# Performance work log

Measured on AMD Instinct MI355X. Metric: run time of the kernel, lower is better.

The kernel has to match this reference:

```python
import jax, jax.numpy as jnp
import numpy as np

EMBED_DIM = 1024
N_HEADS = 16
HEAD_DIM = EMBED_DIM // N_HEADS

def setup_inputs() -> dict:
    key = jax.random.key(0)
    kx, kq, kk, kv, ko = jax.random.split(key, 5)
    s = 1.0 / np.sqrt(EMBED_DIM)
    return {
        "x": jax.random.normal(kx, (4, 2048, EMBED_DIM), dtype=jnp.float32),
        "Wq": jax.random.normal(kq, (EMBED_DIM, EMBED_DIM), dtype=jnp.float32) * s,
        "Wk": jax.random.normal(kk, (EMBED_DIM, EMBED_DIM), dtype=jnp.float32) * s,
        "Wv": jax.random.normal(kv, (EMBED_DIM, EMBED_DIM), dtype=jnp.float32) * s,
        "Wo": jax.random.normal(ko, (EMBED_DIM, EMBED_DIM), dtype=jnp.float32) * s,
    }

def reference(x, Wq, Wk, Wv, Wo):
    B, T, D = x.shape
    H, Dh = N_HEADS, HEAD_DIM
    # projections (nn.Linear: y = x @ W.T); split heads -> [B, H, T, Dh]
    Q = (x @ Wq.T).reshape(B, T, H, Dh).transpose(0, 2, 1, 3)
    K = (x @ Wk.T).reshape(B, T, H, Dh).transpose(0, 2, 1, 3)
    V = (x @ Wv.T).reshape(B, T, H, Dh).transpose(0, 2, 1, 3)
    scores = jnp.einsum("bhqd,bhkd->bhqk", Q, K) / jnp.sqrt(jnp.float32(Dh))
    attn = jax.nn.softmax(scores, axis=-1)
    out = jnp.einsum("bhqk,bhkd->bhqd", attn, V)  # [B,H,T,Dh]
    out = out.transpose(0, 2, 1, 3).reshape(B, T, D)
    return out @ Wo.T
```

## Files before the change

### kernel.cpp

```cpp
#include <hip/hip_runtime.h>

typedef _Float16 f16;
typedef _Float16 f16x8 __attribute__((ext_vector_type(8)));
typedef _Float16 f16x4 __attribute__((ext_vector_type(4)));
typedef float f32x4 __attribute__((ext_vector_type(4)));

#define MFMA16(a, b, c) __builtin_amdgcn_mfma_f32_16x16x32_f16((a), (b), (c), 0, 0, 0)
#define MEMBAR() __asm__ __volatile__("" ::: "memory")

__device__ __forceinline__ void cp16(const f16* g, f16* l) {
  __builtin_amdgcn_global_load_lds(
      (const __attribute__((address_space(1))) void*)g,
      (__attribute__((address_space(3))) void*)l, 16, 0, 0);
}

__global__ __launch_bounds__(256) void cvt_all(
    const float* __restrict__ x,  const float* __restrict__ Wq,
    const float* __restrict__ Wk, const float* __restrict__ Wv,
    const float* __restrict__ Wo,
    f16* __restrict__ X16, f16* __restrict__ Wq16, f16* __restrict__ Wk16,
    f16* __restrict__ Wv16, f16* __restrict__ Wo16) {
  int blk = blockIdx.x;
  const float* src; f16* dst; size_t off;
  if (blk < 4096) { src = x; dst = X16; off = (size_t)blk * 2048; }
  else {
    int t = blk - 4096, widx = t >> 9, loc = t & 511;
    src = (widx == 0) ? Wq : (widx == 1) ? Wk : (widx == 2) ? Wv : Wo;
    dst = (widx == 0) ? Wq16 : (widx == 1) ? Wk16 : (widx == 2) ? Wv16 : Wo16;
    off = (size_t)loc * 2048;
  }
  size_t e = off + (size_t)threadIdx.x * 8;
  const float4* s = (const float4*)(src + e);
  float4 a = s[0], b = s[1];
  f16x8 o;
  o[0] = (f16)a.x; o[1] = (f16)a.y; o[2] = (f16)a.z; o[3] = (f16)a.w;
  o[4] = (f16)b.x; o[5] = (f16)b.y; o[6] = (f16)b.z; o[7] = (f16)b.w;
  *(f16x8*)(dst + e) = o;
}

__device__ __forceinline__ void gemm_core(
    const f16* __restrict__ A, const f16* __restrict__ B, void* __restrict__ Cv,
    bool outF16, bool permT, int N, int K, int bm, int bn, float scale,
    f16* As, f16* Bs) {
  const int tid = threadIdx.x;
  const int lane = tid & 63, w = tid >> 6;
  const int wm = w >> 1, wn = w & 1;
  const int c = lane & 15, q = lane >> 4;
  const int key = (c >> 1) & 3;
  f32x4 acc[4][4] = {};

  const int Lrow = lane >> 2, Lp = (lane & 3) ^ ((lane >> 3) & 3);
  auto stage = [&](int k0, int bufi) {
#pragma unroll
    for (int j = 0; j < 2; ++j) {
      int r0 = (w * 2 + j) * 16;
      cp16(A + (size_t)(bm + r0 + Lrow) * K + k0 + Lp * 8,
           As + bufi * 4096 + r0 * 32 + lane * 8);
    }
#pragma unroll
    for (int j = 0; j < 2; ++j) {
      int r0 = (w * 2 + j) * 16;
      cp16(B + (size_t)(bn + r0 + Lrow) * K + k0 + Lp * 8,
           Bs + bufi * 4096 + r0 * 32 + lane * 8);
    }
  };

  stage(0, 0);
  const int NIT = K >> 5;
  for (int i = 0; i < NIT; ++i) {
    if (i + 1 < NIT) {
      stage((i + 1) << 5, (i + 1) & 1);
      __builtin_amdgcn_s_waitcnt(0x0F74);
    } else {
      __builtin_amdgcn_s_waitcnt(0x0F70);
    }
    __builtin_amdgcn_s_barrier();
    MEMBAR();
    const f16* Ab = As + (i & 1) * 4096;
    const f16* Bb = Bs + (i & 1) * 4096;
    f16x8 af[4], bf[4];
#pragma unroll
    for (int mt = 0; mt < 4; ++mt)
      af[mt] = *(const f16x8*)(Ab + (wm * 64 + mt * 16 + c) * 32 + (q ^ key) * 8);
#pragma unroll
    for (int nt = 0; nt < 4; ++nt)
      bf[nt] = *(const f16x8*)(Bb + (wn * 64 + nt * 16 + c) * 32 + (q ^ key) * 8);
#pragma unroll
    for (int mt = 0; mt < 4; ++mt)
#pragma unroll
      for (int nt = 0; nt < 4; ++nt)
        acc[mt][nt] = MFMA16(af[mt], bf[nt], acc[mt][nt]);
    MEMBAR();
    __builtin_amdgcn_s_barrier();
  }

#pragma unroll
  for (int mt = 0; mt < 4; ++mt)
#pragma unroll
    for (int nt = 0; nt < 4; ++nt)
#pragma unroll
      for (int r = 0; r < 4; ++r) {
        size_t row = bm + wm * 64 + mt * 16 + q * 4 + r;
        size_t col = bn + wn * 64 + nt * 16 + c;
        if (permT) {
          int t = (int)col & 63;
          col = (col & ~(size_t)63) |
                (size_t)((t & 0x23) | ((t & 0x0C) << 1) | ((t & 0x10) >> 2));
        }
        float v = acc[mt][nt][r] * scale;
        if (outF16) ((f16*)Cv)[row * N + col] = (f16)v;
        else ((float*)Cv)[row * N + col] = v;
      }
}

__global__ __launch_bounds__(256, 4) void gemm_qkvt(
    const f16* __restrict__ X, const f16* __restrict__ Wq,
    const f16* __restrict__ Wk, const f16* __restrict__ Wv,
    f16* __restrict__ Q, f16* __restrict__ Ko, f16* __restrict__ VT, float cs) {
  __shared__ __align__(16) f16 As[8192], Bs[8192];
  const int z = blockIdx.z, x = blockIdx.x;
  if (z < 2) {
    gemm_core(X, z ? Wk : Wq, z ? (void*)Ko : (void*)Q, true, false, 1024, 1024,
              (x >> 3) * 128, (x & 7) * 128, z ? 1.0f : cs, As, Bs);
  } else {
    gemm_core(Wv, X, (void*)VT, true, true, 8192, 1024,
              (x >> 6) * 128, (x & 63) * 128, 1.0f, As, Bs);
  }
}

__global__ __launch_bounds__(256, 4) void gemm_o(
    const f16* __restrict__ A, const f16* __restrict__ Wo, float* __restrict__ out) {
  __shared__ __align__(16) f16 As[8192], Bs[8192];
  const int x = blockIdx.x;
  gemm_core(A, Wo, (void*)out, false, false, 1024, 1024,
            (x >> 3) * 128, (x & 7) * 128, 1.0f, As, Bs);
}

__global__ __launch_bounds__(256, 2) void attn_kernel(
    const f16* __restrict__ Qg, const f16* __restrict__ Kg,
    const f16* __restrict__ VTg, f16* __restrict__ Og) {
  const int T = 2048, D = 1024;
  const int x = blockIdx.x;
  const int xcd = x & 7, rem = x >> 3;
  const int qt = rem & 7, grp = rem >> 3;
  const int bh = (grp << 3) | xcd;
  const int b = bh >> 4, h = bh & 15;
  const size_t base = ((size_t)b * T) * D + h * 64;
  const size_t baseV = (size_t)h * 64 * 8192 + (size_t)b * T;
  __shared__ __align__(16) f16 smem[24576];
  const int tid = threadIdx.x;
  const int lane = tid & 63, w = tid >> 6;
  const int c = lane & 15, q = lane >> 4;
  const int cx = c & 7;
  f16* Kb = smem;
  f16* Vb = smem + 12288;

#pragma unroll
  for (int j = 0; j < 8; ++j) {
    int cb = (w * 8 + j) * 64;
    int ch = cb + lane;
    int row = ch >> 3, p = (ch & 7) ^ (row & 7);
    cp16(Qg + base + (size_t)(qt * 256 + row) * D + p * 8, smem + cb * 8);
  }
  __syncthreads();
  f16x8 qf[4][2];
#pragma unroll
  for (int g = 0; g < 4; ++g)
#pragma unroll
    for (int kh = 0; kh < 2; ++kh)
      qf[g][kh] = *(const f16x8*)(smem + (w * 64 + g * 16 + c) * 64 + ((kh * 4 + q) ^ cx) * 8);
  __syncthreads();

  float l_[4] = {0.f, 0.f, 0.f, 0.f};
  f32x4 o_[4][4] = {};
  const f32x4 zero4 = {0.f, 0.f, 0.f, 0.f};

  auto stageKV = [&](int kv, int bufi) {
    f16* Ks = Kb + bufi * 4096;
    f16* Vt = Vb + bufi * 4096;
#pragma unroll
    for (int j = 0; j < 2; ++j) {
      int cb = (w * 2 + j) * 64;
      int ch = cb + lane;
      int row = ch >> 3, p = (ch & 7) ^ (row & 7);
      cp16(Kg + base + (size_t)(kv + row) * D + p * 8, Ks + cb * 8);
    }
#pragma unroll
    for (int j = 0; j < 2; ++j) {
      int cb = (w * 2 + j) * 64;
      int ch = cb + lane;
      int row = ch >> 3, p = (ch & 7) ^ (row & 7);
      cp16(VTg + baseV + (size_t)row * 8192 + kv + p * 8, Vt + cb * 8);
    }
  };

  auto loadKF = [&](const f16* Ks, f16x8 kf[2][4]) {
#pragma unroll
    for (int kh = 0; kh < 2; ++kh)
#pragma unroll
      for (int mt = 0; mt < 4; ++mt)
        kf[kh][mt] = *(const f16x8*)(Ks + (mt * 16 + c) * 64 + ((kh * 4 + q) ^ cx) * 8);
  };

  f32x4 st[4][4];

  stageKV(0, 0);
  stageKV(64, 1);
  __builtin_amdgcn_s_waitcnt(0x0F74);
  __builtin_amdgcn_s_barrier();
  MEMBAR();
  {
    f16x8 kf[2][4];
    loadKF(Kb, kf);
    __builtin_amdgcn_s_setprio(1);
#pragma unroll
    for (int mt = 0; mt < 4; ++mt)
#pragma unroll
      for (int g = 0; g < 4; ++g)
        st[mt][g] = MFMA16(kf[0][mt], qf[g][0], zero4);
#pragma unroll
    for (int mt = 0; mt < 4; ++mt)
#pragma unroll
      for (int g = 0; g < 4; ++g)
        st[mt][g] = MFMA16(kf[1][mt], qf[g][1], st[mt][g]);
    __builtin_amdgcn_s_setprio(0);
  }

  for (int i = 0; i < 31; ++i) {
    __builtin_amdgcn_s_waitcnt(0x0F70);
    __builtin_amdgcn_s_barrier();
    MEMBAR();
    if (i < 30) stageKV((i + 2) * 64, (i + 2) % 3);

    f16x8 kf[2][4];
    loadKF(Kb + ((i + 1) % 3) * 4096, kf);

    f16x8 pf[4][2];
#pragma unroll
    for (int g = 0; g < 4; ++g) {
      float s = 0.f;
#pragma unroll
      for (int mt = 0; mt < 4; ++mt) {
        float p0 = __builtin_amdgcn_exp2f(st[mt][g][0]);
        float p1 = __builtin_amdgcn_exp2f(st[mt][g][1]);
        float p2 = __builtin_amdgcn_exp2f(st[mt][g][2]);
        float p3 = __builtin_amdgcn_exp2f(st[mt][g][3]);
        s += (p0 + p1) + (p2 + p3);
        int kc = mt >> 1, hh = (mt & 1) * 4;
        pf[g][kc][hh + 0] = (f16)p0; pf[g][kc][hh + 1] = (f16)p1;
        pf[g][kc][hh + 2] = (f16)p2; pf[g][kc][hh + 3] = (f16)p3;
      }
      l_[g] += s;
    }

    __builtin_amdgcn_s_setprio(1);
#pragma unroll
    for (int mt = 0; mt < 4; ++mt)
#pragma unroll
      for (int g = 0; g < 4; ++g)
        st[mt][g] = MFMA16(kf[0][mt], qf[g][0], zero4);
#pragma unroll
    for (int mt = 0; mt < 4; ++mt)
#pragma unroll
      for (int g = 0; g < 4; ++g)
        st[mt][g] = MFMA16(kf[1][mt], qf[g][1], st[mt][g]);

    const f16* Vt = Vb + (i % 3) * 4096;
#pragma unroll
    for (int kc = 0; kc < 2; ++kc)
#pragma unroll
      for (int d = 0; d < 4; ++d) {
        f16x8 vf = *(const f16x8*)(Vt + (d * 16 + c) * 64 + ((kc * 4 + q) ^ cx) * 8);
        o_[0][d] = MFMA16(pf[0][kc], vf, o_[0][d]);
        o_[1][d] = MFMA16(pf[1][kc], vf, o_[1][d]);
        o_[2][d] = MFMA16(pf[2][kc], vf, o_[2][d]);
        o_[3][d] = MFMA16(pf[3][kc], vf, o_[3][d]);
      }
    __builtin_amdgcn_s_setprio(0);
    MEMBAR();
  }

  {
    f16x8 pf[4][2];
#pragma unroll
    for (int g = 0; g < 4; ++g) {
      float s = 0.f;
#pragma unroll
      for (int mt = 0; mt < 4; ++mt) {
        float p0 = __builtin_amdgcn_exp2f(st[mt][g][0]);
        float p1 = __builtin_amdgcn_exp2f(st[mt][g][1]);
        float p2 = __builtin_amdgcn_exp2f(st[mt][g][2]);
        float p3 = __builtin_amdgcn_exp2f(st[mt][g][3]);
        s += (p0 + p1) + (p2 + p3);
        int kc = mt >> 1, hh = (mt & 1) * 4;
        pf[g][kc][hh + 0] = (f16)p0; pf[g][kc][hh + 1] = (f16)p1;
        pf[g][kc][hh + 2] = (f16)p2; pf[g][kc][hh + 3] = (f16)p3;
      }
      l_[g] += s;
    }
    const f16* Vt = Vb + (31 % 3) * 4096;
    __builtin_amdgcn_s_setprio(1);
#pragma unroll
    for (int kc = 0; kc < 2; ++kc)
#pragma unroll
      for (int d = 0; d < 4; ++d) {
        f16x8 vf = *(const f16x8*)(Vt + (d * 16 + c) * 64 + ((kc * 4 + q) ^ cx) * 8);
        o_[0][d] = MFMA16(pf[0][kc], vf, o_[0][d]);
        o_[1][d] = MFMA16(pf[1][kc], vf, o_[1][d]);
        o_[2][d] = MFMA16(pf[2][kc], vf, o_[2][d]);
        o_[3][d] = MFMA16(pf[3][kc], vf, o_[3][d]);
      }
    __builtin_amdgcn_s_setprio(0);
  }

#pragma unroll
  for (int g = 0; g < 4; ++g) {
    l_[g] += __shfl_xor(l_[g], 16);
    l_[g] += __shfl_xor(l_[g], 32);
  }

#pragma unroll
  for (int g = 0; g < 4; ++g)
#pragma unroll
    for (int r = 0; r < 4; ++r) {
      float linv = 1.0f / __shfl(l_[g], q * 4 + r);
      size_t row = (size_t)qt * 256 + w * 64 + g * 16 + q * 4 + r;
#pragma unroll
      for (int d = 0; d < 4; ++d)
        Og[base + row * D + d * 16 + c] = (f16)(o_[g][d][r] * linv);
    }
}

extern "C" void kernel_launch(void* const* d_in, const int* in_sizes, int n_in,
                              void* d_out, int out_size, void* d_ws, size_t ws_size,
                              hipStream_t stream) {
  const float* x  = (const float*)d_in[0];
  const float* Wq = (const float*)d_in[1];
  const float* Wk = (const float*)d_in[2];
  const float* Wv = (const float*)d_in[3];
  const float* Wo = (const float*)d_in[4];
  char* ws = (char*)d_ws;
  const size_t MB = 1ull << 20;
  f16* X16  = (f16*)(ws + 0 * MB);
  f16* Wq16 = (f16*)(ws + 16 * MB);
  f16* Wk16 = (f16*)(ws + 18 * MB);
  f16* Wv16 = (f16*)(ws + 20 * MB);
  f16* Wo16 = (f16*)(ws + 22 * MB);
  f16* Q16  = (f16*)(ws + 24 * MB);
  f16* K16  = (f16*)(ws + 40 * MB);
  f16* VT16 = (f16*)(ws + 56 * MB);
  f16* A16  = (f16*)(ws + 72 * MB);

  const float cs = 0.18033688011112042f;

  cvt_all<<<6144, 256, 0, stream>>>(x, Wq, Wk, Wv, Wo,
                                    X16, Wq16, Wk16, Wv16, Wo16);

  gemm_qkvt<<<dim3(512, 1, 3), 256, 0, stream>>>(
      X16, Wq16, Wk16, Wv16, Q16, K16, VT16, cs);

  attn_kernel<<<dim3(512, 1, 1), 256, 0, stream>>>(Q16, K16, VT16, A16);

  gemm_o<<<512, 256, 0, stream>>>(A16, Wo16, (float*)d_out);
}
```

Baseline: 259.6 us.

## Interleave per-group softmax exp with QK and PV MFMAs, preload V fragments

Restructures the attention inner loop so the exp/sum/convert work for query group g+1 runs between the MFMA bursts for group g, rather than doing all softmax first and then all MFMAs. V fragments are loaded from LDS up front. Conversion to f16 now uses packed round-toward-zero cvt_pkrtz. The goal is to overlap VALU transcendental work with matrix-core execution and cut conversion instructions. In exchange, register pressure rises from the hoisted vf array, rounding changes from nearest to toward-zero, and setprio toggles more often.

Result: slower. 310.0 us (+19.4%).

```diff
diff --git a/kernel.cpp b/kernel.cpp
--- a/kernel.cpp
+++ b/kernel.cpp
@@ -3,6 +3,7 @@
 typedef _Float16 f16;
 typedef _Float16 f16x8 __attribute__((ext_vector_type(8)));
 typedef _Float16 f16x4 __attribute__((ext_vector_type(4)));
+typedef __fp16 h16x2 __attribute__((ext_vector_type(2)));
 typedef float f32x4 __attribute__((ext_vector_type(4)));
 
 #define MFMA16(a, b, c) __builtin_amdgcn_mfma_f32_16x16x32_f16((a), (b), (c), 0, 0, 0)
@@ -203,6 +204,23 @@
   };
 
   f32x4 st[4][4];
+  union U8 { f16x8 v; h16x2 h[4]; };
+  U8 pf[4][2];
+
+  auto doSM = [&](int g) {
+    float s = 0.f;
+#pragma unroll
+    for (int mt = 0; mt < 4; ++mt) {
+      float p0 = __builtin_amdgcn_exp2f(st[mt][g][0]);
+      float p1 = __builtin_amdgcn_exp2f(st[mt][g][1]);
+      float p2 = __builtin_amdgcn_exp2f(st[mt][g][2]);
+      float p3 = __builtin_amdgcn_exp2f(st[mt][g][3]);
+      s += (p0 + p1) + (p2 + p3);
+      pf[g][mt >> 1].h[(mt & 1) * 2 + 0] = __builtin_amdgcn_cvt_pkrtz(p0, p1);
+      pf[g][mt >> 1].h[(mt & 1) * 2 + 1] = __builtin_amdgcn_cvt_pkrtz(p2, p3);
+    }
+    l_[g] += s;
+  };
 
   stageKV(0, 0);
   stageKV(64, 1);
@@ -234,83 +252,55 @@
 
     f16x8 kf[2][4];
     loadKF(Kb + ((i + 1) % 3) * 4096, kf);
-
-    f16x8 pf[4][2];
+    const f16* Vt = Vb + (i % 3) * 4096;
+    f16x8 vf[2][4];
+#pragma unroll
+    for (int kc = 0; kc < 2; ++kc)
+#pragma unroll
+      for (int d = 0; d < 4; ++d)
+        vf[kc][d] = *(const f16x8*)(Vt + (d * 16 + c) * 64 + ((kc * 4 + q) ^ cx) * 8);
+
+    doSM(0);
 #pragma unroll
     for (int g = 0; g < 4; ++g) {
-      float s = 0.f;
-#pragma unroll
-      for (int mt = 0; mt < 4; ++mt) {
-        float p0 = __builtin_amdgcn_exp2f(st[mt][g][0]);
-        float p1 = __builtin_amdgcn_exp2f(st[mt][g][1]);
-        float p2 = __builtin_amdgcn_exp2f(st[mt][g][2]);
-        float p3 = __builtin_amdgcn_exp2f(st[mt][g][3]);
-        s += (p0 + p1) + (p2 + p3);
-        int kc = mt >> 1, hh = (mt & 1) * 4;
-        pf[g][kc][hh + 0] = (f16)p0; pf[g][kc][hh + 1] = (f16)p1;
-        pf[g][kc][hh + 2] = (f16)p2; pf[g][kc][hh + 3] = (f16)p3;
-      }
-      l_[g] += s;
-    }
-
-    __builtin_amdgcn_s_setprio(1);
-#pragma unroll
-    for (int mt = 0; mt < 4; ++mt)
-#pragma unroll
-      for (int g = 0; g < 4; ++g)
+      __builtin_amdgcn_s_setprio(1);
+#pragma unroll
+      for (int mt = 0; mt < 4; ++mt)
         st[mt][g] = MFMA16(kf[0][mt], qf[g][0], zero4);
 #pragma unroll
-    for (int mt = 0; mt < 4; ++mt)
-#pragma unroll
-      for (int g = 0; g < 4; ++g)
+      for (int mt = 0; mt < 4; ++mt)
         st[mt][g] = MFMA16(kf[1][mt], qf[g][1], st[mt][g]);
-
-    const f16* Vt = Vb + (i % 3) * 4096;
+#pragma unroll
+      for (int kc = 0; kc < 2; ++kc)
+#pragma unroll
+        for (int d = 0; d < 4; ++d)
+          o_[g][d] = MFMA16(pf[g][kc].v, vf[kc][d], o_[g][d]);
+      __builtin_amdgcn_s_setprio(0);
+      if (g < 3) doSM(g + 1);
+    }
+    MEMBAR();
+  }
+
+  {
+    const f16* Vt = Vb + (31 % 3) * 4096;
+    f16x8 vf[2][4];
 #pragma unroll
     for (int kc = 0; kc < 2; ++kc)
 #pragma unroll
-      for (int d = 0; d < 4; ++d) {
-        f16x8 vf = *(const f16x8*)(Vt + (d * 16 + c) * 64 + ((kc * 4 + q) ^ cx) * 8);
-        o_[0][d] = MFMA16(pf[0][kc], vf, o_[0][d]);
-        o_[1][d] = MFMA16(pf[1][kc], vf, o_[1][d]);
-        o_[2][d] = MFMA16(pf[2][kc], vf, o_[2][d]);
-        o_[3][d] = MFMA16(pf[3][kc], vf, o_[3][d]);
-      }
-    __builtin_amdgcn_s_setprio(0);
-    MEMBAR();
-  }
-
-  {
-    f16x8 pf[4][2];
+      for (int d = 0; d < 4; ++d)
+        vf[kc][d] = *(const f16x8*)(Vt + (d * 16 + c) * 64 + ((kc * 4 + q) ^ cx) * 8);
+    doSM(0);
 #pragma unroll
     for (int g = 0; g < 4; ++g) {
-      float s = 0.f;
-#pragma unroll
-      for (int mt = 0; mt < 4; ++mt) {
-        float p0 = __builtin_amdgcn_exp2f(st[mt][g][0]);
-        float p1 = __builtin_amdgcn_exp2f(st[mt][g][1]);
-        float p2 = __builtin_amdgcn_exp2f(st[mt][g][2]);
-        float p3 = __builtin_amdgcn_exp2f(st[mt][g][3]);
-        s += (p0 + p1) + (p2 + p3);
-        int kc = mt >> 1, hh = (mt & 1) * 4;
-        pf[g][kc][hh + 0] = (f16)p0; pf[g][kc][hh + 1] = (f16)p1;
-        pf[g][kc][hh + 2] = (f16)p2; pf[g][kc][hh + 3] = (f16)p3;
-      }
-      l_[g] += s;
-    }
-    const f16* Vt = Vb + (31 % 3) * 4096;
-    __builtin_amdgcn_s_setprio(1);
-#pragma unroll
-    for (int kc = 0; kc < 2; ++kc)
-#pragma unroll
-      for (int d = 0; d < 4; ++d) {
-        f16x8 vf = *(const f16x8*)(Vt + (d * 16 + c) * 64 + ((kc * 4 + q) ^ cx) * 8);
-        o_[0][d] = MFMA16(pf[0][kc], vf, o_[0][d]);
-        o_[1][d] = MFMA16(pf[1][kc], vf, o_[1][d]);
-        o_[2][d] = MFMA16(pf[2][kc], vf, o_[2][d]);
-        o_[3][d] = MFMA16(pf[3][kc], vf, o_[3][d]);
-      }
-    __builtin_amdgcn_s_setprio(0);
+      __builtin_amdgcn_s_setprio(1);
+#pragma unroll
+      for (int kc = 0; kc < 2; ++kc)
+#pragma unroll
+        for (int d = 0; d < 4; ++d)
+          o_[g][d] = MFMA16(pf[g][kc].v, vf[kc][d], o_[g][d]);
+      __builtin_amdgcn_s_setprio(0);
+      if (g < 3) doSM(g + 1);
+    }
   }
 
 #pragma unroll
```
